# Optimization experiments

Hardware: AMD Instinct MI355X
Metric: run time of the kernel (lower is better)

The kernel has to match this reference:

```python
import jax, jax.numpy as jnp
import numpy as np

L = 5   # num GIN layers
D = 128 # input_dim == hidden_dim
BN_EPS = 1e-5

def _bn(x, g, b):
    # training-mode BatchNorm1d over nodes: biased variance, eps=1e-5
    m = jnp.mean(x, axis=0)
    v = jnp.var(x, axis=0)
    return g * (x - m) * jax.lax.rsqrt(v + BN_EPS) + b

def setup_inputs() -> dict:
    key = jax.random.key(0)
    ks = jax.random.split(key, 12)
    N, E = 50000, 800000
    h = jax.random.normal(ks[0], (N, D), dtype=jnp.float32)
    src = jax.random.randint(ks[1], (E,), 0, N)
    dst = jax.random.randint(ks[2], (E,), 0, N)
    s = 1.0 / np.sqrt(D)
    W1 = jax.random.uniform(ks[3], (L, D, D), jnp.float32, -s, s)
    b1 = jax.random.uniform(ks[4], (L, D), jnp.float32, -s, s)
    W2 = jax.random.uniform(ks[5], (L, D, D), jnp.float32, -s, s)
    b2 = jax.random.uniform(ks[6], (L, D), jnp.float32, -s, s)
    bn1_g = jax.random.uniform(ks[7], (L, D), jnp.float32, 0.5, 1.5)
    bn1_b = jax.random.normal(ks[8], (L, D), jnp.float32) * 0.1
    bn2_g = jax.random.uniform(ks[9], (L, D), jnp.float32, 0.5, 1.5)
    bn2_b = jax.random.normal(ks[10], (L, D), jnp.float32) * 0.1
    bn3_g = jax.random.uniform(ks[11], (L, D), jnp.float32, 0.5, 1.5)
    bn3_b = jnp.zeros((L, D), jnp.float32)
    return dict(h=h, src=src, dst=dst, W1=W1, b1=b1, W2=W2, b2=b2,
                bn1_g=bn1_g, bn1_b=bn1_b, bn2_g=bn2_g, bn2_b=bn2_b,
                bn3_g=bn3_g, bn3_b=bn3_b)

def reference(h, src, dst, W1, b1, W2, b2, bn1_g, bn1_b, bn2_g, bn2_b, bn3_g, bn3_b):
    N = h.shape[0]
    for l in range(L):
        # GINConv, sum aggregation, eps = 0: (1+eps)*h + sum_{j->i} h_j
        agg = jax.ops.segment_sum(h[src], dst, num_segments=N)
        rst = h + agg
        # MLP: linear -> BN -> ReLU -> linear (linear output)
        x = rst @ W1[l] + b1[l]
        x = jax.nn.relu(_bn(x, bn1_g[l], bn1_b[l]))
        x = x @ W2[l] + b2[l]
        # ApplyNodeFunc: BN + ReLU
        x = jax.nn.relu(_bn(x, bn2_g[l], bn2_b[l]))
        # GIN outer BatchNorm + ReLU
        h = jax.nn.relu(_bn(x, bn3_g[l], bn3_b[l]))
    return h
```

## Files before the change

kernel.cpp:

```cpp
#include <hip/hip_runtime.h>
#include <hip/hip_bf16.h>
#include <cstdint>

#define BN_EPS 1e-5f

typedef __attribute__((ext_vector_type(8))) short short8;
typedef __attribute__((ext_vector_type(8))) __bf16 bf16x8;
typedef __attribute__((ext_vector_type(4))) float f32x4;

__device__ inline short f2bf(float f) {
    union { float f; unsigned u; } v; v.f = f;
    unsigned r = v.u + 0x7fffu + ((v.u >> 16) & 1u);
    return (short)(r >> 16);
}
__device__ inline float bf2f(short h) {
    union { unsigned u; float f; } v;
    v.u = ((unsigned)(unsigned short)h) << 16;
    return v.f;
}


__global__ void zero_kernel(float* stats, int nstats, int* deg, int N) {
    int i = blockIdx.x * 256 + threadIdx.x;
    if (i < nstats) stats[i] = 0.f;
    if (i < N) deg[i] = 0;
}

__global__ void h2bf_kernel(const float* __restrict__ h, unsigned short* __restrict__ hb,
                            int total4) {
    int i = blockIdx.x * 256 + threadIdx.x;
    if (i >= total4) return;
    float4 v = ((const float4*)h)[i];
    ushort4 o;
    o.x = (unsigned short)f2bf(v.x);
    o.y = (unsigned short)f2bf(v.y);
    o.z = (unsigned short)f2bf(v.z);
    o.w = (unsigned short)f2bf(v.w);
    ((ushort4*)hb)[i] = o;
}

__global__ void tw_kernel(const float* __restrict__ W1, const float* __restrict__ W2,
                          short* __restrict__ WtHi, short* __restrict__ WtLo) {
    int t = blockIdx.x * 256 + threadIdx.x;
    if (t >= 10 * 128 * 128) return;
    int mat = t >> 14, n = (t >> 7) & 127, k = t & 127;
    const float* W = (mat < 5) ? (W1 + mat * 16384) : (W2 + (mat - 5) * 16384);
    float w = W[k * 128 + n];
    short hi = f2bf(w);
    WtHi[t] = hi;
    WtLo[t] = f2bf(w - bf2f(hi));
}

__global__ void count_kernel(const int* __restrict__ dst, int* __restrict__ deg, int E) {
    int e = blockIdx.x * 256 + threadIdx.x;
    if (e < E) atomicAdd(&deg[dst[e]], 1);
}


__global__ __launch_bounds__(256) void scanA_kernel(const int* __restrict__ deg,
                                                    int* __restrict__ blockSums, int N) {
    int t = threadIdx.x, b = blockIdx.x;
    int base = b * 1024 + t * 4;
    int s = 0;
#pragma unroll
    for (int k = 0; k < 4; ++k) { int i = base + k; if (i < N) s += deg[i]; }
#pragma unroll
    for (int off = 1; off < 64; off <<= 1) s += __shfl_xor(s, off, 64);
    __shared__ int ws[4];
    if ((t & 63) == 0) ws[t >> 6] = s;
    __syncthreads();
    if (t == 0) blockSums[b] = ws[0] + ws[1] + ws[2] + ws[3];
}

__global__ __launch_bounds__(256) void scanB_kernel(int* __restrict__ blockSums,
                                                    int* __restrict__ rowptrN, int nb) {
    __shared__ int ps[256];
    int t = threadIdx.x;
    int v = (t < nb) ? blockSums[t] : 0;
    ps[t] = v;
    __syncthreads();
#pragma unroll
    for (int off = 1; off < 256; off <<= 1) {
        int u = 0;
        if (t >= off) u = ps[t - off];
        __syncthreads();
        ps[t] += u;
        __syncthreads();
    }
    if (t < nb) blockSums[t] = ps[t] - v;
    if (t == 255) rowptrN[0] = ps[255];
}

__global__ __launch_bounds__(256) void scanC_kernel(const int* __restrict__ deg,
                                                    const int* __restrict__ blockSums,
                                                    int* __restrict__ rowptr,
                                                    int* __restrict__ cursor, int N) {
    __shared__ int ps[256];
    int t = threadIdx.x, b = blockIdx.x;
    int base = b * 1024 + t * 4;
    int d[4];
    int s = 0;
#pragma unroll
    for (int k = 0; k < 4; ++k) {
        d[k] = (base + k < N) ? deg[base + k] : 0;
        s += d[k];
    }
    int local = s;
    ps[t] = s;
    __syncthreads();
#pragma unroll
    for (int off = 1; off < 256; off <<= 1) {
        int u = 0;
        if (t >= off) u = ps[t - off];
        __syncthreads();
        ps[t] += u;
        __syncthreads();
    }
    int pre = ps[t] - local + blockSums[b];
#pragma unroll
    for (int k = 0; k < 4; ++k) {
        int i = base + k;
        if (i < N) { rowptr[i] = pre; cursor[i] = pre; pre += d[k]; }
    }
}

__global__ void fill_kernel(const int* __restrict__ src, const int* __restrict__ dst,
                            int* __restrict__ cursor, int* __restrict__ colidx, int E) {
    int e = blockIdx.x * 256 + threadIdx.x;
    if (e < E) {
        int p = atomicAdd(&cursor[dst[e]], 1);
        colidx[p] = src[e];
    }
}

__device__ inline void coeff_from_stats(const float* __restrict__ stats,
                                        const float* __restrict__ g,
                                        const float* __restrict__ bb,
                                        int col, int N, float& a, float& c) {
    float s = 0.f, q = 0.f;
#pragma unroll
    for (int st = 0; st < 8; ++st) {
        s += stats[st * 256 + col];
        q += stats[st * 256 + 128 + col];
    }
    float m = s / N, v = q / N - m * m;
    a = g[col] * rsqrtf(v + BN_EPS);
    c = bb[col] - m * a;
}


template <int MODE>
__global__ __launch_bounds__(256) void agg_kernel(
    const unsigned short* __restrict__ Xb, const int* __restrict__ rowptr,
    const int* __restrict__ colidx,
    const float* __restrict__ stats2, const float* __restrict__ g2, const float* __restrict__ b2v,
    const float* __restrict__ stats3, const float* __restrict__ g3, const float* __restrict__ b3v,
    float* __restrict__ rst, int N) {
    __shared__ float cf[4][128];
    int t = threadIdx.x;
    if (MODE) {
        if (t < 128) {
            float a, c;
            coeff_from_stats(stats2, g2, b2v, t, N, a, c);
            cf[0][t] = a; cf[1][t] = c;
            coeff_from_stats(stats3, g3, b3v, t, N, a, c);
            cf[2][t] = a; cf[3][t] = c;
        }
        __syncthreads();
    }
    int node = (blockIdx.x * 256 + t) >> 6;
    if (node >= N) return;
    int lane = t & 63;
    int c0 = lane * 2, c1 = c0 + 1;
    float a2x = 1.f, c2x = 0.f, a2y = 1.f, c2y = 0.f;
    float a3x = 1.f, c3x = 0.f, a3y = 1.f, c3y = 0.f;
    if (MODE) {
        a2x = cf[0][c0]; a2y = cf[0][c1]; c2x = cf[1][c0]; c2y = cf[1][c1];
        a3x = cf[2][c0]; a3y = cf[2][c1]; c3x = cf[3][c0]; c3y = cf[3][c1];
    }
    auto fx = [&](float u) {
        if (MODE == 0) return u;
        float z = fmaxf(a2x * u + c2x, 0.f);
        return fmaxf(a3x * z + c3x, 0.f);
    };
    auto fy = [&](float u) {
        if (MODE == 0) return u;
        float z = fmaxf(a2y * u + c2y, 0.f);
        return fmaxf(a3y * z + c3y, 0.f);
    };
    const ushort2* X2 = (const ushort2*)Xb;
    ushort2 self = X2[(size_t)node * 64 + lane];
    float ax = fx(bf2f((short)self.x)), ay = fy(bf2f((short)self.y));
    int e = rowptr[node], end = rowptr[node + 1];
    for (; e + 8 <= end; e += 8) {
        int j[8];
#pragma unroll
        for (int k = 0; k < 8; ++k) j[k] = colidx[e + k];
        ushort2 v[8];
#pragma unroll
        for (int k = 0; k < 8; ++k) v[k] = X2[(size_t)j[k] * 64 + lane];
#pragma unroll
        for (int k = 0; k < 8; ++k) {
            ax += fx(bf2f((short)v[k].x));
            ay += fy(bf2f((short)v[k].y));
        }
    }
    for (; e < end; ++e) {
        int j = colidx[e];
        ushort2 v = X2[(size_t)j * 64 + lane];
        ax += fx(bf2f((short)v.x));
        ay += fy(bf2f((short)v.y));
    }
    float2 r; r.x = ax; r.y = ay;
    ((float2*)rst)[(size_t)node * 64 + lane] = r;
}


template <int PRE, int OUTBF>
__global__ __launch_bounds__(256, 2) void gemm_kernel(
    const float* __restrict__ A,
    const short* __restrict__ WtHi, const short* __restrict__ WtLo,
    const float* __restrict__ bias,
    const float* __restrict__ preStats, const float* __restrict__ preG,
    const float* __restrict__ preB,
    float* __restrict__ C, unsigned short* __restrict__ Cb,
    float* __restrict__ outStats, int N) {
    __shared__ short WsHi[128 * 128];
    __shared__ short WsLo[128 * 128];

    const int t = threadIdx.x;
    const int row0 = blockIdx.x * 128;
    const int w = t >> 6, lane = t & 63;
    const int quad = lane >> 4, l16 = lane & 15;
    const int sw = (l16 & 7) * 8;

    float aE = 1.f, cE = 0.f, aO = 1.f, cO = 0.f;
    if (PRE) {
        coeff_from_stats(preStats, preG, preB, lane * 2, N, aE, cE);
        coeff_from_stats(preStats, preG, preB, lane * 2 + 1, N, aO, cO);
    }

    float4 af[2][4][2];
#pragma unroll
    for (int m = 0; m < 2; ++m) {
        int gr = row0 + w * 32 + m * 16 + l16;
        bool ok = gr < N;
        const float* Ar = A + (size_t)gr * 128;
#pragma unroll
        for (int kk = 0; kk < 4; ++kk) {
            int kb = kk * 32 + quad * 8;
            af[m][kk][0] = ok ? *(const float4*)(Ar + kb) : make_float4(0.f, 0.f, 0.f, 0.f);
            af[m][kk][1] = ok ? *(const float4*)(Ar + kb + 4) : make_float4(0.f, 0.f, 0.f, 0.f);
        }
    }

#pragma unroll
    for (int i = 0; i < 8; ++i) {
        int ch = t + i * 256;
        int r = ch >> 4, k = (ch & 15) * 8;
        int d = r * 128 + (k ^ ((r & 7) * 8));
        *(short8*)(WsHi + d) = *(const short8*)(WtHi + r * 128 + k);
        *(short8*)(WsLo + d) = *(const short8*)(WtLo + r * 128 + k);
    }
    __syncthreads();

    short8 fh[2][4], fl[2][4];
#pragma unroll
    for (int kk = 0; kk < 4; ++kk) {
        float a8[8], c8[8];
#pragma unroll
        for (int j = 0; j < 8; ++j) {
            if (PRE) {
                int col = kk * 32 + quad * 8 + j;
                int srcl = col >> 1;
                a8[j] = __shfl((j & 1) ? aO : aE, srcl, 64);
                c8[j] = __shfl((j & 1) ? cO : cE, srcl, 64);
            }
        }
#pragma unroll
        for (int m = 0; m < 2; ++m) {
            float x[8];
            *(float4*)(x) = af[m][kk][0];
            *(float4*)(x + 4) = af[m][kk][1];
            short8 h, lo;
#pragma unroll
            for (int j = 0; j < 8; ++j) {
                float y = PRE ? fmaxf(a8[j] * x[j] + c8[j], 0.f) : x[j];
                short hi = f2bf(y);
                h[j] = hi;
                lo[j] = f2bf(y - bf2f(hi));
            }
            fh[m][kk] = h;
            fl[m][kk] = lo;
        }
    }

    f32x4 acc[2][8];
#pragma unroll
    for (int m = 0; m < 2; ++m)
#pragma unroll
        for (int n = 0; n < 8; ++n) acc[m][n] = (f32x4){0.f, 0.f, 0.f, 0.f};

#pragma unroll
    for (int kk = 0; kk < 4; ++kk) {
        int kb = kk * 32 + quad * 8;
        bf16x8 a0h = __builtin_bit_cast(bf16x8, fh[0][kk]);
        bf16x8 a1h = __builtin_bit_cast(bf16x8, fh[1][kk]);
        bf16x8 a0l = __builtin_bit_cast(bf16x8, fl[0][kk]);
        bf16x8 a1l = __builtin_bit_cast(bf16x8, fl[1][kk]);
#pragma unroll
        for (int n = 0; n < 8; ++n) {
            int woff = (n * 16 + l16) * 128 + (kb ^ sw);
            bf16x8 bh = __builtin_bit_cast(bf16x8, *(const short8*)(WsHi + woff));
            bf16x8 bl = __builtin_bit_cast(bf16x8, *(const short8*)(WsLo + woff));
            acc[0][n] = __builtin_amdgcn_mfma_f32_16x16x32_bf16(a0h, bh, acc[0][n], 0, 0, 0);
            acc[0][n] = __builtin_amdgcn_mfma_f32_16x16x32_bf16(a0l, bh, acc[0][n], 0, 0, 0);
            acc[0][n] = __builtin_amdgcn_mfma_f32_16x16x32_bf16(a0h, bl, acc[0][n], 0, 0, 0);
            acc[1][n] = __builtin_amdgcn_mfma_f32_16x16x32_bf16(a1h, bh, acc[1][n], 0, 0, 0);
            acc[1][n] = __builtin_amdgcn_mfma_f32_16x16x32_bf16(a1l, bh, acc[1][n], 0, 0, 0);
            acc[1][n] = __builtin_amdgcn_mfma_f32_16x16x32_bf16(a1h, bl, acc[1][n], 0, 0, 0);
        }
    }

    __syncthreads();

    float bv[8];
#pragma unroll
    for (int n = 0; n < 8; ++n) bv[n] = bias[n * 16 + l16];
    float ls[8], lsq[8];
#pragma unroll
    for (int n = 0; n < 8; ++n) { ls[n] = 0.f; lsq[n] = 0.f; }
#pragma unroll
    for (int m = 0; m < 2; ++m) {
        int rbase = row0 + w * 32 + m * 16 + quad * 4;
#pragma unroll
        for (int n = 0; n < 8; ++n) {
            int colv = n * 16 + l16;
#pragma unroll
            for (int r = 0; r < 4; ++r) {
                int row = rbase + r;
                if (row < N) {
                    float val = acc[m][n][r] + bv[n];
                    if (OUTBF) {
                        short hb = f2bf(val);
                        float vr = bf2f(hb);
                        Cb[(size_t)row * 128 + colv] = (unsigned short)hb;
                        ls[n] += vr;
                        lsq[n] += vr * vr;
                    } else {
                        C[(size_t)row * 128 + colv] = val;
                        ls[n] += val;
                        lsq[n] += val * val;
                    }
                }
            }
        }
    }

    float* P = (float*)WsHi;
#pragma unroll
    for (int n = 0; n < 8; ++n) {
        float s = ls[n], q = lsq[n];
        s += __shfl_xor(s, 16, 64);
        s += __shfl_xor(s, 32, 64);
        q += __shfl_xor(q, 16, 64);
        q += __shfl_xor(q, 32, 64);
        if (quad == 0) {
            int colv = n * 16 + l16;
            P[w * 512 + colv] = s;
            P[w * 512 + 256 + colv] = q;
        }
    }
    __syncthreads();

    int stripe = blockIdx.x & 7;
    if (t < 128) {
        int col = t;
        float S = P[col] + P[512 + col] + P[1024 + col] + P[1536 + col];
        atomicAdd(&outStats[stripe * 256 + col], S);
    } else {
        int col = t - 128;
        float Q = P[256 + col] + P[768 + col] + P[1280 + col] + P[1792 + col];
        atomicAdd(&outStats[stripe * 256 + 128 + col], Q);
    }
}


__global__ __launch_bounds__(256) void elt_kernel(
    const unsigned short* __restrict__ Xb,
    const float* __restrict__ inStats, const float* __restrict__ g, const float* __restrict__ bb,
    float* __restrict__ outStats, int N) {
    __shared__ float red[256 * 8];
    __shared__ float cf[2][128];
    int t = threadIdx.x;
    if (t < 128) {
        float a, c;
        coeff_from_stats(inStats, g, bb, t, N, a, c);
        cf[0][t] = a; cf[1][t] = c;
    }
    __syncthreads();
    int cg = t & 31;
    float a[4], c[4];
#pragma unroll
    for (int k = 0; k < 4; ++k) {
        a[k] = cf[0][cg * 4 + k];
        c[k] = cf[1][cg * 4 + k];
    }
    float sum[4] = {0.f, 0.f, 0.f, 0.f}, sq[4] = {0.f, 0.f, 0.f, 0.f};
    int total = N * 32;
    for (int i = blockIdx.x * 256 + t; i < total; i += gridDim.x * 256) {
        ushort4 u = ((const ushort4*)Xb)[i];
        float y0 = fmaxf(a[0] * bf2f((short)u.x) + c[0], 0.f);
        float y1 = fmaxf(a[1] * bf2f((short)u.y) + c[1], 0.f);
        float y2 = fmaxf(a[2] * bf2f((short)u.z) + c[2], 0.f);
        float y3 = fmaxf(a[3] * bf2f((short)u.w) + c[3], 0.f);
        sum[0] += y0; sq[0] += y0 * y0;
        sum[1] += y1; sq[1] += y1 * y1;
        sum[2] += y2; sq[2] += y2 * y2;
        sum[3] += y3; sq[3] += y3 * y3;
    }
#pragma unroll
    for (int k = 0; k < 4; ++k) { red[t * 8 + k] = sum[k]; red[t * 8 + 4 + k] = sq[k]; }
    __syncthreads();
    if (t < 32) {
        float S[4] = {0.f, 0.f, 0.f, 0.f}, Q[4] = {0.f, 0.f, 0.f, 0.f};
        for (int j = 0; j < 8; ++j) {
            int tt = t + 32 * j;
#pragma unroll
            for (int k = 0; k < 4; ++k) { S[k] += red[tt * 8 + k]; Q[k] += red[tt * 8 + 4 + k]; }
        }
        int stripe = blockIdx.x & 7;
#pragma unroll
        for (int k = 0; k < 4; ++k) {
            atomicAdd(&outStats[stripe * 256 + t * 4 + k], S[k]);
            atomicAdd(&outStats[stripe * 256 + 128 + t * 4 + k], Q[k]);
        }
    }
}


__global__ __launch_bounds__(256) void final_kernel(
    const unsigned short* __restrict__ Xb,
    const float* __restrict__ stats2, const float* __restrict__ g2, const float* __restrict__ b2v,
    const float* __restrict__ stats3, const float* __restrict__ g3, const float* __restrict__ b3v,
    float* __restrict__ out, int N) {
    __shared__ float cf[4][128];
    int t = threadIdx.x;
    if (t < 128) {
        float a, c;
        coeff_from_stats(stats2, g2, b2v, t, N, a, c);
        cf[0][t] = a; cf[1][t] = c;
        coeff_from_stats(stats3, g3, b3v, t, N, a, c);
        cf[2][t] = a; cf[3][t] = c;
    }
    __syncthreads();
    int cg = t & 31;
    float a2[4], c2[4], a3[4], c3[4];
#pragma unroll
    for (int k = 0; k < 4; ++k) {
        int colv = cg * 4 + k;
        a2[k] = cf[0][colv]; c2[k] = cf[1][colv];
        a3[k] = cf[2][colv]; c3[k] = cf[3][colv];
    }
    int total = N * 32;
    for (int i = blockIdx.x * 256 + t; i < total; i += gridDim.x * 256) {
        ushort4 u = ((const ushort4*)Xb)[i];
        float4 y;
        y.x = fmaxf(a3[0] * fmaxf(a2[0] * bf2f((short)u.x) + c2[0], 0.f) + c3[0], 0.f);
        y.y = fmaxf(a3[1] * fmaxf(a2[1] * bf2f((short)u.y) + c2[1], 0.f) + c3[1], 0.f);
        y.z = fmaxf(a3[2] * fmaxf(a2[2] * bf2f((short)u.z) + c2[2], 0.f) + c3[2], 0.f);
        y.w = fmaxf(a3[3] * fmaxf(a2[3] * bf2f((short)u.w) + c2[3], 0.f) + c3[3], 0.f);
        ((float4*)out)[i] = y;
    }
}


extern "C" void kernel_launch(void* const* d_in, const int* in_sizes, int n_in,
                              void* d_out, int out_size, void* d_ws, size_t ws_size,
                              hipStream_t stream) {
    const float* h0   = (const float*)d_in[0];
    const int*   src  = (const int*)d_in[1];
    const int*   dst  = (const int*)d_in[2];
    const float* W1   = (const float*)d_in[3];
    const float* b1   = (const float*)d_in[4];
    const float* W2   = (const float*)d_in[5];
    const float* b2   = (const float*)d_in[6];
    const float* bn1g = (const float*)d_in[7];
    const float* bn1b = (const float*)d_in[8];
    const float* bn2g = (const float*)d_in[9];
    const float* bn2b = (const float*)d_in[10];
    const float* bn3g = (const float*)d_in[11];
    const float* bn3b = (const float*)d_in[12];
    const int N = in_sizes[0] / 128;
    const int E = in_sizes[1];

    char* ws = (char*)d_ws;
    size_t off = 0;
    auto alloc = [&](size_t bytes) {
        void* p = ws + off;
        off = (off + bytes + 255) & ~(size_t)255;
        return p;
    };
    float* stats   = (float*)alloc((size_t)5 * 3 * 8 * 256 * sizeof(float));
    int*   deg     = (int*)alloc((size_t)N * 4);
    int*   cursor  = (int*)alloc((size_t)N * 4);
    int*   rowptr  = (int*)alloc((size_t)(N + 1) * 4);
    int*   colidx  = (int*)alloc((size_t)E * 4);
    int*   bsums   = (int*)alloc(1024);
    short* WtHi    = (short*)alloc((size_t)10 * 16384 * 2);
    short* WtLo    = (short*)alloc((size_t)10 * 16384 * 2);
    float* buf0    = (float*)alloc((size_t)N * 128 * 4);
    float* buf1    = (float*)alloc((size_t)N * 128 * 4);
    unsigned short* xbf = (unsigned short*)alloc((size_t)N * 128 * 2);

    auto statsBase = [&](int l, int which) { return stats + ((size_t)(l * 3 + which)) * 8 * 256; };

    const int nstats = 5 * 3 * 8 * 256;
    int zgrid = ((N > nstats ? N : nstats) + 255) / 256;
    zero_kernel<<<zgrid, 256, 0, stream>>>(stats, nstats, deg, N);
    h2bf_kernel<<<(N * 32 + 255) / 256, 256, 0, stream>>>(h0, xbf, N * 32);
    tw_kernel<<<(10 * 16384 + 255) / 256, 256, 0, stream>>>(W1, W2, WtHi, WtLo);
    count_kernel<<<(E + 255) / 256, 256, 0, stream>>>(dst, deg, E);
    int nb = (N + 1023) / 1024;
    scanA_kernel<<<nb, 256, 0, stream>>>(deg, bsums, N);
    scanB_kernel<<<1, 256, 0, stream>>>(bsums, rowptr + N, nb);
    scanC_kernel<<<nb, 256, 0, stream>>>(deg, bsums, rowptr, cursor, N);
    fill_kernel<<<(E + 255) / 256, 256, 0, stream>>>(src, dst, cursor, colidx, E);

    const int gemmGrid = (N + 127) / 128;
    const int aggGrid = (N + 3) / 4;
    for (int l = 0; l < 5; ++l) {
        if (l == 0) {
            agg_kernel<0><<<aggGrid, 256, 0, stream>>>(
                xbf, rowptr, colidx,
                nullptr, nullptr, nullptr, nullptr, nullptr, nullptr,
                buf0, N);
        } else {
            int lp = l - 1;
            agg_kernel<1><<<aggGrid, 256, 0, stream>>>(
                xbf, rowptr, colidx,
                statsBase(lp, 1), bn2g + lp * 128, bn2b + lp * 128,
                statsBase(lp, 2), bn3g + lp * 128, bn3b + lp * 128,
                buf0, N);
        }
        gemm_kernel<0, 0><<<gemmGrid, 256, 0, stream>>>(
            buf0, WtHi + l * 16384, WtLo + l * 16384, b1 + l * 128,
            nullptr, nullptr, nullptr,
            buf1, nullptr, statsBase(l, 0), N);
        gemm_kernel<1, 1><<<gemmGrid, 256, 0, stream>>>(
            buf1, WtHi + (5 + l) * 16384, WtLo + (5 + l) * 16384, b2 + l * 128,
            statsBase(l, 0), bn1g + l * 128, bn1b + l * 128,
            nullptr, xbf, statsBase(l, 1), N);
        elt_kernel<<<256, 256, 0, stream>>>(
            xbf, statsBase(l, 1), bn2g + l * 128, bn2b + l * 128,
            statsBase(l, 2), N);
    }
    final_kernel<<<512, 256, 0, stream>>>(
        xbf,
        statsBase(4, 1), bn2g + 4 * 128, bn2b + 4 * 128,
        statsBase(4, 2), bn3g + 4 * 128, bn3b + 4 * 128,
        (float*)d_out, N);
}
```

Measured before the change: 655.2 us.

## Build CSR via two-level bucket sort, widen gather unroll, use perm for bf16 split

Replaces the per-node global-atomic degree count, three-pass scan and atomic fill with a bucketed build. Edges are histogrammed by 128-node bucket in shared memory, scattered as (src,dst) pairs into bucket ranges, then each bucket block builds rowptr and colidx with LDS atomics. This is meant to cut contended global atomics and random writes. The aggregation loop now unrolls by 16 with a 4-wide tail, and the GEMM's hi/lo bf16 split uses byte-permute and masking instead of round-to-nearest conversion, which changes rounding to truncation for the hi part.

```diff
diff --git a/kernel.cpp b/kernel.cpp
--- a/kernel.cpp
+++ b/kernel.cpp
@@ -3,6 +3,8 @@
 #include <cstdint>
 
 #define BN_EPS 1e-5f
+#define CSR_SHIFT 7
+#define NBMAX 512
 
 typedef __attribute__((ext_vector_type(8))) short short8;
 typedef __attribute__((ext_vector_type(8))) __bf16 bf16x8;
@@ -18,12 +20,14 @@
     v.u = ((unsigned)(unsigned short)h) << 16;
     return v.f;
 }
-
-
-__global__ void zero_kernel(float* stats, int nstats, int* deg, int N) {
+__device__ inline unsigned asu(float f) { union { float f; unsigned u; } v; v.f = f; return v.u; }
+__device__ inline float asf(unsigned u) { union { unsigned u; float f; } v; v.u = u; return v.f; }
+
+
+__global__ void zero_kernel(float* stats, int nstats, int* bcnt, int nb) {
     int i = blockIdx.x * 256 + threadIdx.x;
     if (i < nstats) stats[i] = 0.f;
-    if (i < N) deg[i] = 0;
+    if (i < nb) bcnt[i] = 0;
 }
 
 __global__ void h2bf_kernel(const float* __restrict__ h, unsigned short* __restrict__ hb,
@@ -51,85 +55,106 @@
     WtLo[t] = f2bf(w - bf2f(hi));
 }
 
-__global__ void count_kernel(const int* __restrict__ dst, int* __restrict__ deg, int E) {
-    int e = blockIdx.x * 256 + threadIdx.x;
-    if (e < E) atomicAdd(&deg[dst[e]], 1);
-}
-
-
-__global__ __launch_bounds__(256) void scanA_kernel(const int* __restrict__ deg,
-                                                    int* __restrict__ blockSums, int N) {
-    int t = threadIdx.x, b = blockIdx.x;
-    int base = b * 1024 + t * 4;
-    int s = 0;
-#pragma unroll
-    for (int k = 0; k < 4; ++k) { int i = base + k; if (i < N) s += deg[i]; }
-#pragma unroll
-    for (int off = 1; off < 64; off <<= 1) s += __shfl_xor(s, off, 64);
-    __shared__ int ws[4];
-    if ((t & 63) == 0) ws[t >> 6] = s;
-    __syncthreads();
-    if (t == 0) blockSums[b] = ws[0] + ws[1] + ws[2] + ws[3];
-}
-
-__global__ __launch_bounds__(256) void scanB_kernel(int* __restrict__ blockSums,
-                                                    int* __restrict__ rowptrN, int nb) {
-    __shared__ int ps[256];
+
+__global__ __launch_bounds__(256) void bcount_kernel(const int* __restrict__ dst,
+                                                     int* __restrict__ bucketCnt,
+                                                     int E, int nb, int chunk) {
+    __shared__ int hist[NBMAX];
     int t = threadIdx.x;
-    int v = (t < nb) ? blockSums[t] : 0;
+    for (int i = t; i < nb; i += 256) hist[i] = 0;
+    __syncthreads();
+    int s = blockIdx.x * chunk, e = s + chunk; if (e > E) e = E;
+    for (int i = s + t; i < e; i += 256) atomicAdd(&hist[dst[i] >> CSR_SHIFT], 1);
+    __syncthreads();
+    for (int i = t; i < nb; i += 256) if (hist[i]) atomicAdd(&bucketCnt[i], hist[i]);
+}
+
+__global__ __launch_bounds__(512) void bscan_kernel(const int* __restrict__ bucketCnt,
+                                                    int* __restrict__ bucketBase,
+                                                    int* __restrict__ bucketCursor,
+                                                    int* __restrict__ rowptr,
+                                                    int nb, int N, int E) {
+    __shared__ int ps[NBMAX];
+    int t = threadIdx.x;
+    int v = (t < nb) ? bucketCnt[t] : 0;
     ps[t] = v;
     __syncthreads();
 #pragma unroll
-    for (int off = 1; off < 256; off <<= 1) {
+    for (int off = 1; off < NBMAX; off <<= 1) {
         int u = 0;
         if (t >= off) u = ps[t - off];
         __syncthreads();
         ps[t] += u;
         __syncthreads();
     }
-    if (t < nb) blockSums[t] = ps[t] - v;
-    if (t == 255) rowptrN[0] = ps[255];
-}
-
-__global__ __launch_bounds__(256) void scanC_kernel(const int* __restrict__ deg,
-                                                    const int* __restrict__ blockSums,
-                                                    int* __restrict__ rowptr,
-                                                    int* __restrict__ cursor, int N) {
-    __shared__ int ps[256];
-    int t = threadIdx.x, b = blockIdx.x;
-    int base = b * 1024 + t * 4;
-    int d[4];
-    int s = 0;
-#pragma unroll
-    for (int k = 0; k < 4; ++k) {
-        d[k] = (base + k < N) ? deg[base + k] : 0;
-        s += d[k];
-    }
-    int local = s;
-    ps[t] = s;
-    __syncthreads();
-#pragma unroll
-    for (int off = 1; off < 256; off <<= 1) {
+    if (t < nb) {
+        int b = ps[t] - v;
+        bucketBase[t] = b;
+        bucketCursor[t] = b;
+    }
+    if (t == 0) { bucketBase[nb] = E; rowptr[N] = E; }
+}
+
+__global__ __launch_bounds__(256) void bscatter_kernel(const int* __restrict__ src,
+                                                       const int* __restrict__ dst,
+                                                       int* __restrict__ bucketCursor,
+                                                       uint2* __restrict__ pairs,
+                                                       int E, int nb, int chunk) {
+    __shared__ int cnt[NBMAX];
+    __shared__ int base[NBMAX];
+    int t = threadIdx.x;
+    for (int i = t; i < nb; i += 256) cnt[i] = 0;
+    __syncthreads();
+    int s = blockIdx.x * chunk, e = s + chunk; if (e > E) e = E;
+    for (int i = s + t; i < e; i += 256) atomicAdd(&cnt[dst[i] >> CSR_SHIFT], 1);
+    __syncthreads();
+    for (int i = t; i < nb; i += 256) {
+        int c = cnt[i];
+        base[i] = c ? atomicAdd(&bucketCursor[i], c) : 0;
+    }
+    __syncthreads();
+    for (int i = t; i < nb; i += 256) cnt[i] = 0;
+    __syncthreads();
+    for (int i = s + t; i < e; i += 256) {
+        int d = dst[i];
+        int b = d >> CSR_SHIFT;
+        int slot = atomicAdd(&cnt[b], 1);
+        pairs[base[b] + slot] = make_uint2((unsigned)src[i], (unsigned)d);
+    }
+}
+
+__global__ __launch_bounds__(256) void bbuild_kernel(const uint2* __restrict__ pairs,
+                                                     const int* __restrict__ bucketBase,
+                                                     int* __restrict__ rowptr,
+                                                     int* __restrict__ colidx, int N) {
+    __shared__ int cnt[128];
+    int b = blockIdx.x, t = threadIdx.x;
+    int lo = bucketBase[b], hi = bucketBase[b + 1];
+    if (t < 128) cnt[t] = 0;
+    __syncthreads();
+    for (int e = lo + t; e < hi; e += 256) atomicAdd(&cnt[pairs[e].y & 127], 1);
+    __syncthreads();
+    int orig = (t < 128) ? cnt[t] : 0;
+#pragma unroll
+    for (int o = 1; o < 128; o <<= 1) {
         int u = 0;
-        if (t >= off) u = ps[t - off];
+        if (t < 128 && t >= o) u = cnt[t - o];
         __syncthreads();
-        ps[t] += u;
+        if (t < 128) cnt[t] += u;
         __syncthreads();
     }
-    int pre = ps[t] - local + blockSums[b];
-#pragma unroll
-    for (int k = 0; k < 4; ++k) {
-        int i = base + k;
-        if (i < N) { rowptr[i] = pre; cursor[i] = pre; pre += d[k]; }
-    }
-}
-
-__global__ void fill_kernel(const int* __restrict__ src, const int* __restrict__ dst,
-                            int* __restrict__ cursor, int* __restrict__ colidx, int E) {
-    int e = blockIdx.x * 256 + threadIdx.x;
-    if (e < E) {
-        int p = atomicAdd(&cursor[dst[e]], 1);
-        colidx[p] = src[e];
+    int ex = (t < 128) ? (cnt[t] - orig) : 0;
+    if (t < 128) {
+        int node = b * 128 + t;
+        if (node < N) rowptr[node] = lo + ex;
+    }
+    __syncthreads();
+    if (t < 128) cnt[t] = ex;
+    __syncthreads();
+    for (int e = lo + t; e < hi; e += 256) {
+        uint2 p = pairs[e];
+        int slot = atomicAdd(&cnt[p.y & 127], 1);
+        colidx[lo + slot] = (int)p.x;
     }
 }
 
@@ -192,15 +217,28 @@
     ushort2 self = X2[(size_t)node * 64 + lane];
     float ax = fx(bf2f((short)self.x)), ay = fy(bf2f((short)self.y));
     int e = rowptr[node], end = rowptr[node + 1];
-    for (; e + 8 <= end; e += 8) {
-        int j[8];
-#pragma unroll
-        for (int k = 0; k < 8; ++k) j[k] = colidx[e + k];
-        ushort2 v[8];
-#pragma unroll
-        for (int k = 0; k < 8; ++k) v[k] = X2[(size_t)j[k] * 64 + lane];
-#pragma unroll
-        for (int k = 0; k < 8; ++k) {
+    for (; e + 16 <= end; e += 16) {
+        int j[16];
+#pragma unroll
+        for (int k = 0; k < 16; ++k) j[k] = colidx[e + k];
+        ushort2 v[16];
+#pragma unroll
+        for (int k = 0; k < 16; ++k) v[k] = X2[(size_t)j[k] * 64 + lane];
+#pragma unroll
+        for (int k = 0; k < 16; ++k) {
+            ax += fx(bf2f((short)v[k].x));
+            ay += fy(bf2f((short)v[k].y));
+        }
+    }
+    for (; e + 4 <= end; e += 4) {
+        int j[4];
+#pragma unroll
+        for (int k = 0; k < 4; ++k) j[k] = colidx[e + k];
+        ushort2 v[4];
+#pragma unroll
+        for (int k = 0; k < 4; ++k) v[k] = X2[(size_t)j[k] * 64 + lane];
+#pragma unroll
+        for (int k = 0; k < 4; ++k) {
             ax += fx(bf2f((short)v[k].x));
             ay += fy(bf2f((short)v[k].y));
         }
@@ -284,11 +322,19 @@
             *(float4*)(x + 4) = af[m][kk][1];
             short8 h, lo;
 #pragma unroll
-            for (int j = 0; j < 8; ++j) {
-                float y = PRE ? fmaxf(a8[j] * x[j] + c8[j], 0.f) : x[j];
-                short hi = f2bf(y);
-                h[j] = hi;
-                lo[j] = f2bf(y - bf2f(hi));
+            for (int j = 0; j < 4; ++j) {
+                float x0 = x[2 * j], x1 = x[2 * j + 1];
+                if (PRE) {
+                    x0 = fmaxf(a8[2 * j] * x0 + c8[2 * j], 0.f);
+                    x1 = fmaxf(a8[2 * j + 1] * x1 + c8[2 * j + 1], 0.f);
+                }
+                unsigned u0 = asu(x0), u1 = asu(x1);
+                unsigned hp = __builtin_amdgcn_perm(u1, u0, 0x07060302u);
+                float l0 = x0 - asf(u0 & 0xFFFF0000u);
+                float l1 = x1 - asf(u1 & 0xFFFF0000u);
+                unsigned lp = __builtin_amdgcn_perm(asu(l1), asu(l0), 0x07060302u);
+                ((unsigned*)&h)[j] = hp;
+                ((unsigned*)&lo)[j] = lp;
             }
             fh[m][kk] = h;
             fl[m][kk] = lo;
@@ -493,6 +539,7 @@
     const float* bn3b = (const float*)d_in[12];
     const int N = in_sizes[0] / 128;
     const int E = in_sizes[1];
+    const int nb = (N + 127) >> CSR_SHIFT;
 
     char* ws = (char*)d_ws;
     size_t off = 0;
@@ -501,31 +548,33 @@
         off = (off + bytes + 255) & ~(size_t)255;
         return p;
     };
-    float* stats   = (float*)alloc((size_t)5 * 3 * 8 * 256 * sizeof(float));
-    int*   deg     = (int*)alloc((size_t)N * 4);
-    int*   cursor  = (int*)alloc((size_t)N * 4);
-    int*   rowptr  = (int*)alloc((size_t)(N + 1) * 4);
-    int*   colidx  = (int*)alloc((size_t)E * 4);
-    int*   bsums   = (int*)alloc(1024);
-    short* WtHi    = (short*)alloc((size_t)10 * 16384 * 2);
-    short* WtLo    = (short*)alloc((size_t)10 * 16384 * 2);
-    float* buf0    = (float*)alloc((size_t)N * 128 * 4);
-    float* buf1    = (float*)alloc((size_t)N * 128 * 4);
+    float* stats        = (float*)alloc((size_t)5 * 3 * 8 * 256 * sizeof(float));
+    int*   bucketCnt    = (int*)alloc((size_t)NBMAX * 4);
+    int*   bucketBase   = (int*)alloc((size_t)(NBMAX + 1) * 4);
+    int*   bucketCursor = (int*)alloc((size_t)NBMAX * 4);
+    int*   rowptr       = (int*)alloc((size_t)(N + 1) * 4);
+    int*   colidx       = (int*)alloc((size_t)E * 4);
+    uint2* pairs        = (uint2*)alloc((size_t)E * 8);
+    short* WtHi         = (short*)alloc((size_t)10 * 16384 * 2);
+    short* WtLo         = (short*)alloc((size_t)10 * 16384 * 2);
+    float* buf0         = (float*)alloc((size_t)N * 128 * 4);
+    float* buf1         = (float*)alloc((size_t)N * 128 * 4);
     unsigned short* xbf = (unsigned short*)alloc((size_t)N * 128 * 2);
 
     auto statsBase = [&](int l, int which) { return stats + ((size_t)(l * 3 + which)) * 8 * 256; };
 
     const int nstats = 5 * 3 * 8 * 256;
-    int zgrid = ((N > nstats ? N : nstats) + 255) / 256;
-    zero_kernel<<<zgrid, 256, 0, stream>>>(stats, nstats, deg, N);
+    int zmax = (N > nstats ? N : nstats);
+    zero_kernel<<<(zmax + 255) / 256, 256, 0, stream>>>(stats, nstats, bucketCnt, nb);
     h2bf_kernel<<<(N * 32 + 255) / 256, 256, 0, stream>>>(h0, xbf, N * 32);
     tw_kernel<<<(10 * 16384 + 255) / 256, 256, 0, stream>>>(W1, W2, WtHi, WtLo);
-    count_kernel<<<(E + 255) / 256, 256, 0, stream>>>(dst, deg, E);
-    int nb = (N + 1023) / 1024;
-    scanA_kernel<<<nb, 256, 0, stream>>>(deg, bsums, N);
-    scanB_kernel<<<1, 256, 0, stream>>>(bsums, rowptr + N, nb);
-    scanC_kernel<<<nb, 256, 0, stream>>>(deg, bsums, rowptr, cursor, N);
-    fill_kernel<<<(E + 255) / 256, 256, 0, stream>>>(src, dst, cursor, colidx, E);
+
+    const int chunk = 4096;
+    const int chunkGrid = (E + chunk - 1) / chunk;
+    bcount_kernel<<<chunkGrid, 256, 0, stream>>>(dst, bucketCnt, E, nb, chunk);
+    bscan_kernel<<<1, 512, 0, stream>>>(bucketCnt, bucketBase, bucketCursor, rowptr, nb, N, E);
+    bscatter_kernel<<<chunkGrid, 256, 0, stream>>>(src, dst, bucketCursor, pairs, E, nb, chunk);
+    bbuild_kernel<<<nb, 256, 0, stream>>>(pairs, bucketBase, rowptr, colidx, N);
 
     const int gemmGrid = (N + 127) / 128;
     const int aggGrid = (N + 3) / 4;
```

New measurement: 585.4 us. 10.7% less time.
